# Kernel optimization log

Measured on AMD Instinct MI355X. Metric: run time of the kernel, lower is better.

Reference implementation:

```python
import jax, jax.numpy as jnp
import numpy as np

B = 4096
D = 64  # emb_dim, hardcoded in UserEmb/ItemEmb


def setup_inputs() -> dict:
    key = jax.random.key(0)
    ks = jax.random.split(key, 26)
    n = lambda k, shape, s=1.0: jax.random.normal(k, shape, dtype=jnp.float32) * s
    inp = {
        'user_emb': jax.random.randint(ks[0], (B, 4), 0, 6, dtype=jnp.int32),
        'item_emb': jax.random.randint(ks[1], (B, 10242), 0, 2, dtype=jnp.int32),
        'edge_emb': jnp.zeros((B,), dtype=jnp.int32),  # edges_emb has num_embeddings=1
        # UserEmb params
        'gender_tab': n(ks[2], (98, D)),
        'age_tab': n(ks[3], (7, D)),
        'occ_tab': n(ks[4], (21, D)),
        'area_tab': n(ks[5], (3402, D)),
        'user_W': n(ks[6], (4 * D, D), 0.05),  # stored [in,out]
        'user_b': n(ks[7], (D,), 0.05),
        # ItemEmb params
        'rate_tab': n(ks[8], (6, D)),
        'genre_W': n(ks[9], (25, D), 0.05),
        'director_W': n(ks[10], (2186, D), 0.02),
        'actor_W': n(ks[11], (8030, D), 0.01),
        'item_W': n(ks[12], (4 * D, D), 0.05),
        'item_b': n(ks[13], (D,), 0.05),
        # GLNFeat params (torch: randn * 0.5)
        'edges_tab': n(ks[14], (1, D)),
        'uu_w': n(ks[15], (D,), 0.5),
        'ui_w': n(ks[16], (D,), 0.5),
        'iu_w': n(ks[17], (D,), 0.5),
        'ii_w': n(ks[18], (D,), 0.5),
        'edge_W': n(ks[19], (D, D), 0.5),
        'uu_W1': n(ks[20], (D, D), 0.5),
        'ui_W1': n(ks[21], (D, D), 0.5),
        'iu_W1': n(ks[22], (D, D), 0.5),
        'ii_W1': n(ks[23], (D, D), 0.5),
    }
    return inp


def _lrelu(v):
    return jnp.where(v >= 0, v, 0.01 * v)  # nn.LeakyReLU default slope


def reference(user_emb, item_emb, edge_emb, gender_tab, age_tab, occ_tab, area_tab,
              user_W, user_b, rate_tab, genre_W, director_W, actor_W, item_W, item_b,
              edges_tab, uu_w, ui_w, iu_w, ii_w, edge_W, uu_W1, ui_W1, iu_W1, ii_W1):
    a = 0.12
    b = 0.12
    # UserEmb
    u_cat = jnp.concatenate([gender_tab[user_emb[:, 0]], age_tab[user_emb[:, 1]],
                             occ_tab[user_emb[:, 2]], area_tab[user_emb[:, 3]]], axis=1)
    x = (u_cat @ user_W + user_b) * a  # [B, D]
    # ItemEmb: multi-hot fields projected then mean-normalized by count
    genre = item_emb[:, 1:26].astype(jnp.float32)
    director = item_emb[:, 26:2212].astype(jnp.float32)
    actor = item_emb[:, 2212:10242].astype(jnp.float32)
    ge = (genre @ genre_W) / jnp.sum(genre, 1, keepdims=True)
    de = (director @ director_W) / jnp.sum(director, 1, keepdims=True)
    ae = (actor @ actor_W) / jnp.sum(actor, 1, keepdims=True)
    i_cat = jnp.concatenate([rate_tab[item_emb[:, 0]], ge, de, ae], axis=1)
    y = (i_cat @ item_W + item_b) * a  # [B, D]
    edge = edges_tab[edge_emb] * b  # [B, D]

    def outer_mm(u, v, M):
        # stop_gradient(outer(u, v) @ M) == u[:,None] * (v @ M), avoids [B,B]
        return jax.lax.stop_gradient(u[:, None] * (v @ M))

    xe = x * edge
    ye = y * edge
    x_xx = xe @ uu_w      # [B]
    x_xy_x = xe @ ui_w
    x_xy_y = ye @ ui_w
    t1 = outer_mm(x_xx, x_xx, x)
    t2 = outer_mm(x_xy_x, x_xy_y, y)
    x_buy = (_lrelu(t1 @ uu_W1) + _lrelu(t2 @ ui_W1)) / 2
    y_yy = ye @ ii_w
    y_yx_y = ye @ iu_w
    y_yx_x = xe @ iu_w
    t3 = outer_mm(y_yy, y_yy, y)
    t4 = outer_mm(y_yx_y, y_yx_x, x)
    y_buy = (_lrelu(t3 @ ii_W1) + _lrelu(t4 @ iu_W1)) / 2
    new = _lrelu(edge @ edge_W)
    return ((x_buy + x) / 2, (y_buy + y) / 2, (new + edge) / 2)
```

## Files before the change

kernel.cpp:

```cpp
#include <hip/hip_runtime.h>
#include <cstddef>

constexpr int BATCH = 4096;
constexpr int ITEM_COLS = 10242;
constexpr int FBTK = 10304;
constexpr int NPART = 15;

constexpr int R_GENDER = 0;
constexpr int R_AGE    = 98;
constexpr int R_OCC    = 105;
constexpr int R_AREA   = 126;
constexpr int R_RATE   = 3528;
constexpr int R_FU     = 3534;

constexpr size_t OFF_FU  = 0;
constexpr size_t OFF_NEW = OFF_FU + (size_t)R_FU * 64;
constexpr size_t OFF_FBT = OFF_NEW + 64;
constexpr size_t OFF_X   = OFF_FBT + (size_t)64 * FBTK / 2;
constexpr size_t OFF_Y   = OFF_X + (size_t)BATCH * 64;
constexpr size_t OFF_P   = OFF_Y + (size_t)BATCH * 64;
constexpr size_t OFF_C   = OFF_P + (size_t)NPART * BATCH * 64;
constexpr size_t OFF_SP  = OFF_C + (size_t)NPART * BATCH;
constexpr size_t OFF_PB  = OFF_SP + 256ull * 256;
constexpr size_t OFF_SC  = OFF_PB + 4ull * 64;

__device__ const int AST[NPART] = {0, 24, 792, 1560, 2208, 2976, 3744, 4512, 5280, 6048, 6816, 7584, 8352, 9120, 9888};
__device__ const int VS [NPART] = {0, 25, 792, 1560, 2211, 2976, 3744, 4512, 5280, 6048, 6816, 7584, 8352, 9120, 9888};
__device__ const int VE [NPART] = {25, 792, 1560, 2211, 2976, 3744, 4512, 5280, 6048, 6816, 7584, 8352, 9120, 9888, 10241};
__device__ const int PLEN[NPART] = {128, 768, 768, 768, 768, 768, 768, 768, 768, 768, 768, 768, 768, 768, 384};

typedef __attribute__((ext_vector_type(8))) short bf16x8;
typedef __attribute__((ext_vector_type(4))) float f32x4;

__device__ __forceinline__ float lrelu(float v) { return v >= 0.0f ? v : 0.01f * v; }

__device__ __forceinline__ unsigned bf_rne_pair(float lo, float hi) {
    unsigned ul = __builtin_bit_cast(unsigned, lo);
    unsigned uh = __builtin_bit_cast(unsigned, hi);
    ul += 0x7fffu + ((ul >> 16) & 1u);
    uh += 0x7fffu + ((uh >> 16) & 1u);
    return (ul >> 16) | (uh & 0xffff0000u);
}

__global__ __launch_bounds__(256) void k_fuse(
        const float* __restrict__ gender_tab, const float* __restrict__ age_tab,
        const float* __restrict__ occ_tab, const float* __restrict__ area_tab,
        const float* __restrict__ user_W, const float* __restrict__ rate_tab,
        const float* __restrict__ genre_W, const float* __restrict__ director_W,
        const float* __restrict__ actor_W, const float* __restrict__ item_W,
        const float* __restrict__ edges_tab, const float* __restrict__ edge_W,
        float* __restrict__ Fu, float* __restrict__ NEWt, short* __restrict__ Fbt) {
    const int t = threadIdx.x;
    const int bx = blockIdx.x;
    if (bx < 884) {
        int n = t & 63;
        int rb = __builtin_amdgcn_readfirstlane(t >> 6);
        int r = bx * 4 + rb;
        if (r > R_FU) return;
        if (r == R_FU) {
            float acc = 0.0f;
#pragma unroll
            for (int k = 0; k < 64; ++k)
                acc = fmaf(edges_tab[k] * 0.12f, edge_W[k * 64 + n], acc);
            NEWt[n] = lrelu(acc);
            return;
        }
        const float* src;
        const float* W;
        if (r < R_AGE)       { src = gender_tab + (size_t)r * 64;            W = user_W;            }
        else if (r < R_OCC)  { src = age_tab    + (size_t)(r - R_AGE) * 64;  W = user_W + 64 * 64;  }
        else if (r < R_AREA) { src = occ_tab    + (size_t)(r - R_OCC) * 64;  W = user_W + 128 * 64; }
        else if (r < R_RATE) { src = area_tab   + (size_t)(r - R_AREA) * 64; W = user_W + 192 * 64; }
        else                 { src = rate_tab   + (size_t)(r - R_RATE) * 64; W = item_W;            }
        float acc = 0.0f;
#pragma unroll
        for (int k = 0; k < 64; ++k)
            acc = fmaf(src[k], W[k * 64 + n], acc);
        Fu[(size_t)r * 64 + n] = acc;
        return;
    }
    const int KT0 = (bx - 884) * 64;
    const int n = t & 63;
    const int rb = __builtin_amdgcn_readfirstlane(t >> 6);
    __shared__ float T[64 * 65];
    for (int rl = 0; rl < 16; ++rl) {
        int r = rl * 4 + rb;
        int KT = KT0 + r;
        float acc = 0.0f;
        if (KT < 10241) {
            const float* src;
            const float* W;
            if (KT < 25)        { src = genre_W    + (size_t)KT * 64;          W = item_W + 64 * 64;  }
            else if (KT < 2211) { src = director_W + (size_t)(KT - 25) * 64;   W = item_W + 128 * 64; }
            else                { src = actor_W    + (size_t)(KT - 2211) * 64; W = item_W + 192 * 64; }
#pragma unroll
            for (int k = 0; k < 64; ++k)
                acc = fmaf(src[k], W[k * 64 + n], acc);
        }
        T[r * 65 + n] = acc;
    }
    __syncthreads();
    int n2 = t >> 2, sg = t & 3;
    unsigned dw[8];
#pragma unroll
    for (int d = 0; d < 8; ++d)
        dw[d] = bf_rne_pair(T[(sg * 16 + 2 * d) * 65 + n2], T[(sg * 16 + 2 * d + 1) * 65 + n2]);
    uint4* dst = (uint4*)(Fbt + (size_t)n2 * FBTK + KT0 + sg * 16);
    dst[0] = make_uint4(dw[0], dw[1], dw[2], dw[3]);
    dst[1] = make_uint4(dw[4], dw[5], dw[6], dw[7]);
}

__global__ __launch_bounds__(256) void k_item(const int* __restrict__ item,
                                              const short* __restrict__ Fbt,
                                              float* __restrict__ P, float* __restrict__ C) {
    const int part = blockIdx.y;
    const int ast = AST[part], vs = VS[part], ve = VE[part], len = PLEN[part];
    const int m0 = blockIdx.x * 64;
    const int t = threadIdx.x;
    const int lane = t & 63;
    const int w = __builtin_amdgcn_readfirstlane(t >> 6);
    const int q = lane >> 4, r16 = lane & 15;

    __shared__ short As[64 * 136];

    f32x4 acc[5];
#pragma unroll
    for (int s = 0; s < 5; ++s) acc[s] = (f32x4){0.f, 0.f, 0.f, 0.f};

    const short o = (r16 == 0) ? (short)0x3f80 : (short)0;
    const bf16x8 ones = {o, o, o, o, o, o, o, o};

    for (int kb = 0; kb < len; kb += 128) {
        __syncthreads();
        const int K0 = ast + kb;
        if (K0 >= vs && K0 + 128 <= ve) {
#pragma unroll
            for (int it = 0; it < 32; ++it) {
                int f = it * 256 + t;
                int r = f >> 7, cc = f & 127;
                int v = item[(size_t)(m0 + r) * ITEM_COLS + 1 + K0 + cc];
                As[r * 136 + cc] = v ? (short)0x3f80 : (short)0;
            }
        } else {
#pragma unroll
            for (int it = 0; it < 32; ++it) {
                int f = it * 256 + t;
                int r = f >> 7, cc = f & 127;
                int KT = K0 + cc;
                int v = (KT >= vs && KT < ve) ? item[(size_t)(m0 + r) * ITEM_COLS + 1 + KT] : 0;
                As[r * 136 + cc] = v ? (short)0x3f80 : (short)0;
            }
        }
        __syncthreads();
        const short* fb = Fbt + K0 + (size_t)q * 8;
#pragma unroll
        for (int kt = 0; kt < 4; ++kt) {
            bf16x8 a = *(const bf16x8*)(As + (w * 16 + r16) * 136 + kt * 32 + q * 8);
#pragma unroll
            for (int s = 0; s < 4; ++s) {
                bf16x8 b = *(const bf16x8*)(fb + (size_t)(s * 16 + r16) * FBTK + kt * 32);
                acc[s] = __builtin_amdgcn_mfma_f32_16x16x32_bf16(a, b, acc[s], 0, 0, 0);
            }
            acc[4] = __builtin_amdgcn_mfma_f32_16x16x32_bf16(a, ones, acc[4], 0, 0, 0);
        }
    }
    const size_t pb = (size_t)part * BATCH + m0 + w * 16 + q * 4;
#pragma unroll
    for (int reg = 0; reg < 4; ++reg) {
        float* pr = P + (pb + reg) * 64 + r16;
        pr[0] = acc[0][reg];
        pr[16] = acc[1][reg];
        pr[32] = acc[2][reg];
        pr[48] = acc[3][reg];
    }
    if (r16 == 0) {
#pragma unroll
        for (int reg = 0; reg < 4; ++reg)
            C[(size_t)part * BATCH + m0 + w * 16 + q * 4 + reg] = acc[4][reg];
    }
}

__device__ __forceinline__ float wred(float v) {
#pragma unroll
    for (int m = 1; m < 64; m <<= 1) v += __shfl_xor(v, m, 64);
    return v;
}

__global__ __launch_bounds__(256) void k_mid(const int* __restrict__ item, const int* __restrict__ edge_emb,
                                             const int* __restrict__ user_emb,
                                             const float* __restrict__ Fu, const float* __restrict__ user_b,
                                             const float* __restrict__ P, const float* __restrict__ C,
                                             const float* __restrict__ item_b, const float* __restrict__ edges_tab,
                                             const float* __restrict__ uu_w, const float* __restrict__ ui_w,
                                             const float* __restrict__ iu_w, const float* __restrict__ ii_w,
                                             float* __restrict__ X, float* __restrict__ Y,
                                             float* __restrict__ SC, float* __restrict__ SP) {
    const int t = threadIdx.x;
    const int n = t & 63;
    const int wv = __builtin_amdgcn_readfirstlane(t >> 6);
    const float uuw = uu_w[n], uiw = ui_w[n], iuw = iu_w[n], iiw = ii_w[n];
    const float ib = item_b[n], ub = user_b[n];
    const size_t cs = (size_t)BATCH * 64;
    float s1 = 0.0f, s2 = 0.0f, s3 = 0.0f, s4 = 0.0f;

    for (int i = 0; i < 4; ++i) {
        int b = blockIdx.x * 16 + wv * 4 + i;
        const int* ue = user_emb + (size_t)b * 4;
        float x = (Fu[(size_t)(R_GENDER + ue[0]) * 64 + n]
                 + Fu[(size_t)(R_AGE    + ue[1]) * 64 + n]
                 + Fu[(size_t)(R_OCC    + ue[2]) * 64 + n]
                 + Fu[(size_t)(R_AREA   + ue[3]) * 64 + n] + ub) * 0.12f;
        X[(size_t)b * 64 + n] = x;
        int ri = item[(size_t)b * ITEM_COLS];
        size_t base = (size_t)b * 64 + n;
        float sg = P[base], cg = C[b];
        float sd = 0.0f, cd = 0.0f, sa = 0.0f, ca = 0.0f;
#pragma unroll
        for (int p2 = 1; p2 < 4; ++p2)  { sd += P[base + p2 * cs]; cd += C[p2 * BATCH + b]; }
#pragma unroll
        for (int p2 = 4; p2 < 15; ++p2) { sa += P[base + p2 * cs]; ca += C[p2 * BATCH + b]; }
        float y = (Fu[(size_t)(R_RATE + ri) * 64 + n] + sg / cg + sd / cd + sa / ca + ib) * 0.12f;
        Y[(size_t)b * 64 + n] = y;
        float e = edges_tab[(size_t)edge_emb[b] * 64 + n] * 0.12f;
        float xe = x * e, ye = y * e;
        float r1 = wred(xe * uuw);
        float r2 = wred(xe * uiw);
        float r3 = wred(xe * iuw);
        float r4 = wred(ye * uiw);
        float r5 = wred(ye * iiw);
        float r6 = wred(ye * iuw);
        if (n == 0) {
            SC[b] = r1; SC[BATCH + b] = r2; SC[2 * BATCH + b] = r5; SC[3 * BATCH + b] = r6;
        }
        s1 = fmaf(r1, x, s1);
        s2 = fmaf(r4, y, s2);
        s3 = fmaf(r5, y, s3);
        s4 = fmaf(r3, x, s4);
    }
    __shared__ float sp[4][4][64];
    sp[wv][0][n] = s1; sp[wv][1][n] = s2; sp[wv][2][n] = s3; sp[wv][3][n] = s4;
    __syncthreads();
    int i2 = t >> 6;
    float v = sp[0][i2][n] + sp[1][i2][n] + sp[2][i2][n] + sp[3][i2][n];
    SP[(size_t)blockIdx.x * 256 + t] = v;
}

__global__ __launch_bounds__(1024) void k_red(const float* __restrict__ SP,
                                              const float* __restrict__ uu_W1, const float* __restrict__ ui_W1,
                                              const float* __restrict__ iu_W1, const float* __restrict__ ii_W1,
                                              float* __restrict__ PB) {
    int t = threadIdx.x;
    int sub = t >> 8, i = (t >> 6) & 3, n = t & 63;
    float s = 0.0f;
    for (int wb = sub * 64; wb < sub * 64 + 64; ++wb)
        s += SP[(size_t)wb * 256 + i * 64 + n];
    __shared__ float red[4][4][64];
    red[sub][i][n] = s;
    __syncthreads();
    float sv = red[0][i][n] + red[1][i][n] + red[2][i][n] + red[3][i][n];
    __shared__ float sl[4][64];
    if (t < 256) sl[i][n] = sv;
    __syncthreads();
    if (t < 256) {
        const float* W1 = (i == 0) ? uu_W1 : (i == 1) ? ui_W1 : (i == 2) ? ii_W1 : iu_W1;
        float p = 0.0f;
#pragma unroll
        for (int k = 0; k < 64; ++k) p = fmaf(sl[i][k], W1[k * 64 + n], p);
        PB[i * 64 + n] = p;
    }
}

__global__ __launch_bounds__(256) void k_out(const float* __restrict__ X, const float* __restrict__ Y,
                                             const float* __restrict__ SC, const float* __restrict__ PB,
                                             const float* __restrict__ NEWt, const float* __restrict__ edges_tab,
                                             const int* __restrict__ edge_emb, float* __restrict__ out) {
    int t = threadIdx.x;
    int b = blockIdx.x * 4 + (t >> 6);
    int n = t & 63;
    float xx = SC[b], xyx = SC[BATCH + b], yy = SC[2 * BATCH + b], yxy = SC[3 * BATCH + b];
    float p1 = PB[n], p2 = PB[64 + n], p3 = PB[128 + n], p4 = PB[192 + n];
    float x = X[(size_t)b * 64 + n], y = Y[(size_t)b * 64 + n];
    float o1 = ((lrelu(xx * p1) + lrelu(xyx * p2)) * 0.5f + x) * 0.5f;
    float o2 = ((lrelu(yy * p3) + lrelu(yxy * p4)) * 0.5f + y) * 0.5f;
    float e = edges_tab[(size_t)edge_emb[b] * 64 + n] * 0.12f;
    float o3 = (NEWt[n] + e) * 0.5f;
    out[(size_t)b * 64 + n] = o1;
    out[((size_t)BATCH + b) * 64 + n] = o2;
    out[((size_t)2 * BATCH + b) * 64 + n] = o3;
}

extern "C" void kernel_launch(void* const* d_in, const int* in_sizes, int n_in,
                              void* d_out, int out_size, void* d_ws, size_t ws_size,
                              hipStream_t stream) {
    (void)in_sizes; (void)n_in; (void)out_size; (void)ws_size;
    const int*   user_emb   = (const int*)  d_in[0];
    const int*   item_emb   = (const int*)  d_in[1];
    const int*   edge_emb   = (const int*)  d_in[2];
    const float* gender_tab = (const float*)d_in[3];
    const float* age_tab    = (const float*)d_in[4];
    const float* occ_tab    = (const float*)d_in[5];
    const float* area_tab   = (const float*)d_in[6];
    const float* user_W     = (const float*)d_in[7];
    const float* user_b     = (const float*)d_in[8];
    const float* rate_tab   = (const float*)d_in[9];
    const float* genre_W    = (const float*)d_in[10];
    const float* director_W = (const float*)d_in[11];
    const float* actor_W    = (const float*)d_in[12];
    const float* item_W     = (const float*)d_in[13];
    const float* item_b     = (const float*)d_in[14];
    const float* edges_tab  = (const float*)d_in[15];
    const float* uu_w       = (const float*)d_in[16];
    const float* ui_w       = (const float*)d_in[17];
    const float* iu_w       = (const float*)d_in[18];
    const float* ii_w       = (const float*)d_in[19];
    const float* edge_W     = (const float*)d_in[20];
    const float* uu_W1      = (const float*)d_in[21];
    const float* ui_W1      = (const float*)d_in[22];
    const float* iu_W1      = (const float*)d_in[23];
    const float* ii_W1      = (const float*)d_in[24];

    float* ws   = (float*)d_ws;
    float* Fu   = ws + OFF_FU;
    float* NEWt = ws + OFF_NEW;
    short* Fbt  = (short*)(ws + OFF_FBT);
    float* X    = ws + OFF_X;
    float* Y    = ws + OFF_Y;
    float* P    = ws + OFF_P;
    float* C    = ws + OFF_C;
    float* SP   = ws + OFF_SP;
    float* PB   = ws + OFF_PB;
    float* SC   = ws + OFF_SC;
    float* out  = (float*)d_out;

    hipLaunchKernelGGL(k_fuse, dim3(884 + FBTK / 64), dim3(256), 0, stream,
                       gender_tab, age_tab, occ_tab, area_tab, user_W, rate_tab,
                       genre_W, director_W, actor_W, item_W, edges_tab, edge_W, Fu, NEWt, Fbt);
    hipLaunchKernelGGL(k_item, dim3(BATCH / 64, NPART), dim3(256), 0, stream, item_emb, Fbt, P, C);
    hipLaunchKernelGGL(k_mid, dim3(BATCH / 16), dim3(256), 0, stream,
                       item_emb, edge_emb, user_emb, Fu, user_b, P, C, item_b, edges_tab,
                       uu_w, ui_w, iu_w, ii_w, X, Y, SC, SP);
    hipLaunchKernelGGL(k_red, dim3(1), dim3(1024), 0, stream, SP, uu_W1, ui_W1, iu_W1, ii_W1, PB);
    hipLaunchKernelGGL(k_out, dim3(BATCH / 4), dim3(256), 0, stream,
                       X, Y, SC, PB, NEWt, edges_tab, edge_emb, out);
}
```

Baseline: 357.7 us.

## Load item multi-hot directly into MFMA registers; replace reduction kernel with atomics

k_item no longer stages the multi-hot item matrix through shared memory with block barriers. Each lane loads its own 8 contiguous ints per k-tile straight from global memory and converts them to bf16 in registers. The separate single-block reduction kernel is removed: k_mid atomically adds its partial sums into a small buffer zeroed in k_fuse, and k_out recomputes the small W1 projection per block before writing outputs. This drops one launch and the serial single-block tail, at the cost of less coalesced global reads in k_item, redundant W1 matvecs in every k_out block, and non-deterministic float atomic summation order.

```diff
diff --git a/kernel.cpp b/kernel.cpp
--- a/kernel.cpp
+++ b/kernel.cpp
@@ -20,9 +20,8 @@
 constexpr size_t OFF_Y   = OFF_X + (size_t)BATCH * 64;
 constexpr size_t OFF_P   = OFF_Y + (size_t)BATCH * 64;
 constexpr size_t OFF_C   = OFF_P + (size_t)NPART * BATCH * 64;
-constexpr size_t OFF_SP  = OFF_C + (size_t)NPART * BATCH;
-constexpr size_t OFF_PB  = OFF_SP + 256ull * 256;
-constexpr size_t OFF_SC  = OFF_PB + 4ull * 64;
+constexpr size_t OFF_S   = OFF_C + (size_t)NPART * BATCH;
+constexpr size_t OFF_SC  = OFF_S + 4ull * 64;
 
 __device__ const int AST[NPART] = {0, 24, 792, 1560, 2208, 2976, 3744, 4512, 5280, 6048, 6816, 7584, 8352, 9120, 9888};
 __device__ const int VS [NPART] = {0, 25, 792, 1560, 2211, 2976, 3744, 4512, 5280, 6048, 6816, 7584, 8352, 9120, 9888};
@@ -49,9 +48,11 @@
         const float* __restrict__ genre_W, const float* __restrict__ director_W,
         const float* __restrict__ actor_W, const float* __restrict__ item_W,
         const float* __restrict__ edges_tab, const float* __restrict__ edge_W,
-        float* __restrict__ Fu, float* __restrict__ NEWt, short* __restrict__ Fbt) {
+        float* __restrict__ Fu, float* __restrict__ NEWt, short* __restrict__ Fbt,
+        float* __restrict__ S) {
     const int t = threadIdx.x;
     const int bx = blockIdx.x;
+    if (bx == 0) S[t] = 0.0f;
     if (bx < 884) {
         int n = t & 63;
         int rb = __builtin_amdgcn_readfirstlane(t >> 6);
@@ -120,8 +121,8 @@
     const int lane = t & 63;
     const int w = __builtin_amdgcn_readfirstlane(t >> 6);
     const int q = lane >> 4, r16 = lane & 15;
-
-    __shared__ short As[64 * 136];
+    const int m = m0 + w * 16 + r16;
+    const int* __restrict__ arow = item + (size_t)m * ITEM_COLS + 1;
 
     f32x4 acc[5];
 #pragma unroll
@@ -131,34 +132,36 @@
     const bf16x8 ones = {o, o, o, o, o, o, o, o};
 
     for (int kb = 0; kb < len; kb += 128) {
-        __syncthreads();
         const int K0 = ast + kb;
+        int va[4][8];
         if (K0 >= vs && K0 + 128 <= ve) {
 #pragma unroll
-            for (int it = 0; it < 32; ++it) {
-                int f = it * 256 + t;
-                int r = f >> 7, cc = f & 127;
-                int v = item[(size_t)(m0 + r) * ITEM_COLS + 1 + K0 + cc];
-                As[r * 136 + cc] = v ? (short)0x3f80 : (short)0;
+            for (int kt = 0; kt < 4; ++kt) {
+                const int* p = arow + K0 + kt * 32 + q * 8;
+#pragma unroll
+                for (int j = 0; j < 8; ++j) va[kt][j] = p[j];
             }
         } else {
 #pragma unroll
-            for (int it = 0; it < 32; ++it) {
-                int f = it * 256 + t;
-                int r = f >> 7, cc = f & 127;
-                int KT = K0 + cc;
-                int v = (KT >= vs && KT < ve) ? item[(size_t)(m0 + r) * ITEM_COLS + 1 + KT] : 0;
-                As[r * 136 + cc] = v ? (short)0x3f80 : (short)0;
+            for (int kt = 0; kt < 4; ++kt) {
+#pragma unroll
+                for (int j = 0; j < 8; ++j) {
+                    int KT = K0 + kt * 32 + q * 8 + j;
+                    int KTc = KT > 10240 ? 10240 : KT;
+                    int v = arow[KTc];
+                    va[kt][j] = (KT >= vs && KT < ve) ? v : 0;
+                }
             }
         }
-        __syncthreads();
-        const short* fb = Fbt + K0 + (size_t)q * 8;
 #pragma unroll
         for (int kt = 0; kt < 4; ++kt) {
-            bf16x8 a = *(const bf16x8*)(As + (w * 16 + r16) * 136 + kt * 32 + q * 8);
+            bf16x8 a;
+#pragma unroll
+            for (int j = 0; j < 8; ++j) a[j] = va[kt][j] ? (short)0x3f80 : (short)0;
+            const short* fb = Fbt + K0 + kt * 32 + q * 8;
 #pragma unroll
             for (int s = 0; s < 4; ++s) {
-                bf16x8 b = *(const bf16x8*)(fb + (size_t)(s * 16 + r16) * FBTK + kt * 32);
+                bf16x8 b = *(const bf16x8*)(fb + (size_t)(s * 16 + r16) * FBTK);
                 acc[s] = __builtin_amdgcn_mfma_f32_16x16x32_bf16(a, b, acc[s], 0, 0, 0);
             }
             acc[4] = __builtin_amdgcn_mfma_f32_16x16x32_bf16(a, ones, acc[4], 0, 0, 0);
@@ -194,7 +197,7 @@
                                              const float* __restrict__ uu_w, const float* __restrict__ ui_w,
                                              const float* __restrict__ iu_w, const float* __restrict__ ii_w,
                                              float* __restrict__ X, float* __restrict__ Y,
-                                             float* __restrict__ SC, float* __restrict__ SP) {
+                                             float* __restrict__ SC, float* __restrict__ S) {
     const int t = threadIdx.x;
     const int n = t & 63;
     const int wv = __builtin_amdgcn_readfirstlane(t >> 6);
@@ -242,51 +245,40 @@
     __syncthreads();
     int i2 = t >> 6;
     float v = sp[0][i2][n] + sp[1][i2][n] + sp[2][i2][n] + sp[3][i2][n];
-    SP[(size_t)blockIdx.x * 256 + t] = v;
-}
-
-__global__ __launch_bounds__(1024) void k_red(const float* __restrict__ SP,
-                                              const float* __restrict__ uu_W1, const float* __restrict__ ui_W1,
-                                              const float* __restrict__ iu_W1, const float* __restrict__ ii_W1,
-                                              float* __restrict__ PB) {
-    int t = threadIdx.x;
-    int sub = t >> 8, i = (t >> 6) & 3, n = t & 63;
-    float s = 0.0f;
-    for (int wb = sub * 64; wb < sub * 64 + 64; ++wb)
-        s += SP[(size_t)wb * 256 + i * 64 + n];
-    __shared__ float red[4][4][64];
-    red[sub][i][n] = s;
-    __syncthreads();
-    float sv = red[0][i][n] + red[1][i][n] + red[2][i][n] + red[3][i][n];
-    __shared__ float sl[4][64];
-    if (t < 256) sl[i][n] = sv;
-    __syncthreads();
-    if (t < 256) {
-        const float* W1 = (i == 0) ? uu_W1 : (i == 1) ? ui_W1 : (i == 2) ? ii_W1 : iu_W1;
-        float p = 0.0f;
-#pragma unroll
-        for (int k = 0; k < 64; ++k) p = fmaf(sl[i][k], W1[k * 64 + n], p);
-        PB[i * 64 + n] = p;
-    }
+    atomicAdd(&S[i2 * 64 + n], v);
 }
 
 __global__ __launch_bounds__(256) void k_out(const float* __restrict__ X, const float* __restrict__ Y,
-                                             const float* __restrict__ SC, const float* __restrict__ PB,
+                                             const float* __restrict__ SC, const float* __restrict__ S,
+                                             const float* __restrict__ uu_W1, const float* __restrict__ ui_W1,
+                                             const float* __restrict__ iu_W1, const float* __restrict__ ii_W1,
                                              const float* __restrict__ NEWt, const float* __restrict__ edges_tab,
                                              const int* __restrict__ edge_emb, float* __restrict__ out) {
-    int t = threadIdx.x;
-    int b = blockIdx.x * 4 + (t >> 6);
-    int n = t & 63;
-    float xx = SC[b], xyx = SC[BATCH + b], yy = SC[2 * BATCH + b], yxy = SC[3 * BATCH + b];
-    float p1 = PB[n], p2 = PB[64 + n], p3 = PB[128 + n], p4 = PB[192 + n];
-    float x = X[(size_t)b * 64 + n], y = Y[(size_t)b * 64 + n];
-    float o1 = ((lrelu(xx * p1) + lrelu(xyx * p2)) * 0.5f + x) * 0.5f;
-    float o2 = ((lrelu(yy * p3) + lrelu(yxy * p4)) * 0.5f + y) * 0.5f;
-    float e = edges_tab[(size_t)edge_emb[b] * 64 + n] * 0.12f;
-    float o3 = (NEWt[n] + e) * 0.5f;
-    out[(size_t)b * 64 + n] = o1;
-    out[((size_t)BATCH + b) * 64 + n] = o2;
-    out[((size_t)2 * BATCH + b) * 64 + n] = o3;
+    const int t = threadIdx.x;
+    const int n = t & 63, i = t >> 6;
+    __shared__ float sS[4][64], sPB[4][64];
+    sS[i][n] = S[i * 64 + n];
+    __syncthreads();
+    const float* W1 = (i == 0) ? uu_W1 : (i == 1) ? ui_W1 : (i == 2) ? ii_W1 : iu_W1;
+    float p = 0.0f;
+#pragma unroll
+    for (int k = 0; k < 64; ++k) p = fmaf(sS[i][k], W1[k * 64 + n], p);
+    sPB[i][n] = p;
+    __syncthreads();
+    const float p1 = sPB[0][n], p2 = sPB[1][n], p3 = sPB[2][n], p4 = sPB[3][n];
+    const float nw = NEWt[n];
+    for (int ii = 0; ii < 4; ++ii) {
+        int b = blockIdx.x * 16 + i * 4 + ii;
+        float xx = SC[b], xyx = SC[BATCH + b], yy = SC[2 * BATCH + b], yxy = SC[3 * BATCH + b];
+        float x = X[(size_t)b * 64 + n], y = Y[(size_t)b * 64 + n];
+        float o1 = ((lrelu(xx * p1) + lrelu(xyx * p2)) * 0.5f + x) * 0.5f;
+        float o2 = ((lrelu(yy * p3) + lrelu(yxy * p4)) * 0.5f + y) * 0.5f;
+        float e = edges_tab[(size_t)edge_emb[b] * 64 + n] * 0.12f;
+        float o3 = (nw + e) * 0.5f;
+        out[(size_t)b * 64 + n] = o1;
+        out[((size_t)BATCH + b) * 64 + n] = o2;
+        out[((size_t)2 * BATCH + b) * 64 + n] = o3;
+    }
 }
 
 extern "C" void kernel_launch(void* const* d_in, const int* in_sizes, int n_in,
@@ -327,19 +319,17 @@
     float* Y    = ws + OFF_Y;
     float* P    = ws + OFF_P;
     float* C    = ws + OFF_C;
-    float* SP   = ws + OFF_SP;
-    float* PB   = ws + OFF_PB;
+    float* S    = ws + OFF_S;
     float* SC   = ws + OFF_SC;
     float* out  = (float*)d_out;
 
     hipLaunchKernelGGL(k_fuse, dim3(884 + FBTK / 64), dim3(256), 0, stream,
                        gender_tab, age_tab, occ_tab, area_tab, user_W, rate_tab,
-                       genre_W, director_W, actor_W, item_W, edges_tab, edge_W, Fu, NEWt, Fbt);
+                       genre_W, director_W, actor_W, item_W, edges_tab, edge_W, Fu, NEWt, Fbt, S);
     hipLaunchKernelGGL(k_item, dim3(BATCH / 64, NPART), dim3(256), 0, stream, item_emb, Fbt, P, C);
     hipLaunchKernelGGL(k_mid, dim3(BATCH / 16), dim3(256), 0, stream,
                        item_emb, edge_emb, user_emb, Fu, user_b, P, C, item_b, edges_tab,
-                       uu_w, ui_w, iu_w, ii_w, X, Y, SC, SP);
-    hipLaunchKernelGGL(k_red, dim3(1), dim3(1024), 0, stream, SP, uu_W1, ui_W1, iu_W1, ii_W1, PB);
-    hipLaunchKernelGGL(k_out, dim3(BATCH / 4), dim3(256), 0, stream,
-                       X, Y, SC, PB, NEWt, edges_tab, edge_emb, out);
-}
+                       uu_w, ui_w, iu_w, ii_w, X, Y, SC, S);
+    hipLaunchKernelGGL(k_out, dim3(BATCH / 16), dim3(256), 0, stream,
+                       X, Y, SC, S, uu_W1, ui_W1, iu_W1, ii_W1, NEWt, edges_tab, edge_emb, out);
+}
```

Result: no change. 360.9 us (+0.9%).
